# Optimization experiments

Measured on AMD Instinct MI355X. Metric: run time of the kernel, lower is better.

Reference implementation:

```python
import jax, jax.numpy as jnp
import numpy as np

N_USERS = 100_000
N_ITEMS = 50_000
N = N_USERS + N_ITEMS
E = 1_000_000
D = 64          # emb_size
H = 4           # head_num
DH = D // H
L_GT = 2
L_GCN = 2


def setup_inputs() -> dict:
    key = jax.random.key(0)
    ks = jax.random.split(key, 8)
    rows = jax.random.randint(ks[0], (E,), 0, N, dtype=jnp.int32)
    cols = jax.random.randint(ks[1], (E,), 0, N, dtype=jnp.int32)
    vals = jax.random.uniform(ks[2], (E,), dtype=jnp.float32)
    user_emb = jax.random.normal(ks[3], (N_USERS, D), dtype=jnp.float32) * 0.1
    item_emb = jax.random.normal(ks[4], (N_ITEMS, D), dtype=jnp.float32) * 0.1
    scale = 1.0 / np.sqrt(D)  # ~xavier
    Wq = jax.random.normal(ks[5], (L_GT, D, D), dtype=jnp.float32) * scale
    Wk = jax.random.normal(ks[6], (L_GT, D, D), dtype=jnp.float32) * scale
    Wv = jax.random.normal(ks[7], (L_GT, D, D), dtype=jnp.float32) * scale
    return {"rows": rows, "cols": cols, "vals": vals,
            "user_emb": user_emb, "item_emb": item_emb,
            "Wq": Wq, "Wk": Wk, "Wv": Wv}


def _spmm(rows, cols, vals, embeds):
    # torch.spmm(adj, embeds) with adj in COO form -> segment-sum over edges
    return jax.ops.segment_sum(vals[:, None] * embeds[cols], rows, num_segments=N)


def _gt_layer(rows, cols, embeds, wq, wk, wv):
    rowE = embeds[rows]                                   # [E, D] gather
    colE = embeds[cols]                                   # [E, D] gather
    q = (rowE @ wq).reshape(E, H, DH)
    k = (colE @ wk).reshape(E, H, DH)
    v = (colE @ wv).reshape(E, H, DH)
    att = jnp.clip(jnp.einsum('ehd,ehd->eh', q, k), -10.0, 10.0)
    expAtt = jnp.exp(att)                                 # [E, H]
    attNorm = jax.ops.segment_sum(expAtt, rows, num_segments=N)[rows]  # scatter-softmax denom
    att = expAtt / (attNorm + 1e-8)
    res = (att[..., None] * v).reshape(E, D)
    return jax.ops.segment_sum(res, rows, num_segments=N)  # [N, D]


def reference(rows, cols, vals, user_emb, item_emb, Wq, Wk, Wv):
    embeds = jnp.concatenate([user_emb, item_emb], axis=0)  # [N, D]
    embeds_lst = [embeds]
    for l in range(L_GT):
        embeds_lst.append(_gt_layer(rows, cols, embeds_lst[-1], Wq[l], Wk[l], Wv[l]))
    for _ in range(L_GCN):
        embeds_lst.append(_spmm(rows, cols, vals, embeds_lst[-1]))
    out = embeds_lst[0]
    for e in embeds_lst[1:]:
        out = out + e
    return out
```

## Files before the change

kernel.cpp:

```cpp
#include <hip/hip_runtime.h>

#define NUSERS 100000
#define NITEMS 50000
#define NTOT   150000
#define NEDGE  1000000
#define NTILE  9375

typedef unsigned int uint32;
typedef unsigned short ushort16;
typedef __attribute__((ext_vector_type(8))) short short8;
typedef __attribute__((ext_vector_type(4))) float f32x4;

__device__ __forceinline__ unsigned short f2bf(float f) {
  unsigned int u = __float_as_uint(f);
  u += 0x7FFFu + ((u >> 16) & 1u);
  return (unsigned short)(u >> 16);
}
__device__ __forceinline__ uint32 pack2bf(float a, float b) {
  return (uint32)f2bf(a) | ((uint32)f2bf(b) << 16);
}
__device__ __forceinline__ float bf_lo(uint32 u) { return __uint_as_float(u << 16); }
__device__ __forceinline__ float bf_hi(uint32 u) { return __uint_as_float(u & 0xFFFF0000u); }

__global__ void k_init(const float* __restrict__ ue, const float* __restrict__ ie,
                       uint32* __restrict__ embb) {
  int i = blockIdx.x * 256 + threadIdx.x;
  if (i >= NTOT * 16) return;
  float4 v = (i < NUSERS * 16) ? ((const float4*)ue)[i]
                               : ((const float4*)ie)[i - NUSERS * 16];
  uint2 pk;
  pk.x = pack2bf(v.x, v.y);
  pk.y = pack2bf(v.z, v.w);
  ((uint2*)embb)[i] = pk;
}

__global__ void k_wpack(const float* __restrict__ Wq, const float* __restrict__ Wk,
                        const float* __restrict__ Wv, uint32* __restrict__ Wbg) {
  int t = blockIdx.x * 256 + threadIdx.x;
  if (t >= 12288) return;
  int l = t / 6144, rem = t % 6144, mat = rem / 2048, j = rem % 2048;
  int n = j >> 5, k2 = j & 31;
  const float* W = (mat == 0 ? Wq : mat == 1 ? Wk : Wv) + l * 4096;
  Wbg[t] = pack2bf(W[k2 * 128 + n], W[k2 * 128 + 64 + n]);
}

__global__ void k_hist(const int* __restrict__ rows, int* __restrict__ cnt,
                       int* __restrict__ rank) {
  int e = blockIdx.x * 256 + threadIdx.x;
  if (e < NEDGE) rank[e] = atomicAdd(&cnt[rows[e]], 1);
}

__global__ void k_scan1(const int* __restrict__ cnt, int* __restrict__ partial,
                        int* __restrict__ blocksums) {
  __shared__ int s[256];
  int t = threadIdx.x, b = blockIdx.x;
  int base = b * 2048 + t * 8;
  int pre[8]; int sum = 0;
  #pragma unroll
  for (int j = 0; j < 8; ++j) {
    int idx = base + j;
    int x = (idx < NTOT) ? cnt[idx] : 0;
    pre[j] = sum; sum += x;
  }
  s[t] = sum; __syncthreads();
  for (int off = 1; off < 256; off <<= 1) {
    int x = (t >= off) ? s[t - off] : 0;
    __syncthreads(); s[t] += x; __syncthreads();
  }
  int excl = s[t] - sum;
  #pragma unroll
  for (int j = 0; j < 8; ++j) {
    int idx = base + j;
    if (idx < NTOT) partial[idx] = excl + pre[j];
  }
  if (t == 255) blocksums[b] = s[255];
}

__global__ void k_scan2(const int* __restrict__ blocksums, int* __restrict__ blockoffs, int nblk) {
  __shared__ int s[128];
  int t = threadIdx.x;
  int x = (t < nblk) ? blocksums[t] : 0;
  s[t] = x; __syncthreads();
  for (int off = 1; off < 128; off <<= 1) {
    int y = (t >= off) ? s[t - off] : 0;
    __syncthreads(); s[t] += y; __syncthreads();
  }
  if (t < nblk) blockoffs[t] = s[t] - x;
}

__global__ void k_scan3(int* __restrict__ row_ptr, const int* __restrict__ blockoffs) {
  int i = blockIdx.x * 256 + threadIdx.x;
  if (i < NTOT) row_ptr[i] += blockoffs[i >> 11];
  if (i == 0) row_ptr[NTOT] = NEDGE;
}

__global__ void k_fill(const int* __restrict__ rows, const int* __restrict__ cols,
                       const float* __restrict__ vals, const int* __restrict__ rank,
                       const int* __restrict__ row_ptr, uint2* __restrict__ epack) {
  int e = blockIdx.x * 256 + threadIdx.x;
  if (e >= NEDGE) return;
  int r = rows[e];
  int pos = row_ptr[r] + rank[e];
  uint2 pk;
  pk.x = (uint32)cols[e];
  pk.y = __float_as_uint(vals[e]);
  epack[pos] = pk;
}

__global__ void __launch_bounds__(256) k_qkv(const uint32* __restrict__ embb,
    const uint32* __restrict__ Wbg, float* __restrict__ Q, uint32* __restrict__ KVb) {
  __shared__ float scr[4][2][16][68];
  int t = threadIdx.x;
  int wave = t >> 6, lane = t & 63;
  int tile = blockIdx.x * 4 + wave;
  if (tile >= NTILE) return;
  int c = lane & 15, quad = lane >> 4;
  int nodeBase = tile * 16;
  const uint32* arow = embb + (nodeBase + c) * 32 + quad * 4;
  uint4 a0u = *(const uint4*)arow;
  uint4 a1u = *(const uint4*)(arow + 16);
  short8 a0 = *(short8*)&a0u;
  short8 a1 = *(short8*)&a1u;
  float (*SK)[68] = scr[wave][0];
  float (*SV)[68] = scr[wave][1];
  const uint32* wbase = Wbg + c * 32 + quad * 4;
  #pragma unroll
  for (int mat = 0; mat < 3; ++mat) {
    f32x4 acc[4];
    #pragma unroll
    for (int nt = 0; nt < 4; ++nt) acc[nt] = (f32x4){0.f, 0.f, 0.f, 0.f};
    const uint32* wb = wbase + mat * 2048;
    #pragma unroll
    for (int nt = 0; nt < 4; ++nt) {
      uint4 b0u = *(const uint4*)(wb + nt * 512);
      uint4 b1u = *(const uint4*)(wb + nt * 512 + 16);
      short8 b0 = *(short8*)&b0u;
      short8 b1 = *(short8*)&b1u;
      acc[nt] = __builtin_amdgcn_mfma_f32_16x16x32_bf16(a0, b0, acc[nt], 0, 0, 0);
      acc[nt] = __builtin_amdgcn_mfma_f32_16x16x32_bf16(a1, b1, acc[nt], 0, 0, 0);
    }
    float (*S)[68] = (mat == 2) ? SV : SK;
    #pragma unroll
    for (int nt = 0; nt < 4; ++nt)
      #pragma unroll
      for (int r = 0; r < 4; ++r)
        S[quad * 4 + r][nt * 16 + c] = acc[nt][r];
    if (mat == 0) {
      #pragma unroll
      for (int i = 0; i < 4; ++i) {
        int node = i * 4 + quad;
        f32x4 q4 = *(f32x4*)&SK[node][c * 4];
        *(f32x4*)&Q[(nodeBase + node) * 64 + c * 4] = q4;
      }
    } else if (mat == 2) {
      #pragma unroll
      for (int i = 0; i < 4; ++i) {
        int node = i * 4 + quad;
        f32x4 K4 = *(f32x4*)&SK[node][c * 4];
        f32x4 V4 = *(f32x4*)&SV[node][c * 4];
        uint4 o;
        o.x = pack2bf(K4[0], K4[1]);
        o.y = pack2bf(K4[2], K4[3]);
        o.z = pack2bf(V4[0], V4[1]);
        o.w = pack2bf(V4[2], V4[3]);
        *(uint4*)&KVb[(nodeBase + node) * 64 + c * 4] = o;
      }
    }
  }
}

__global__ void __launch_bounds__(256) k_gt(const float* __restrict__ Q,
    const uint32* __restrict__ KVb, const int* __restrict__ row_ptr,
    const uint2* __restrict__ epack, float* __restrict__ emb_out,
    uint32* __restrict__ embb_out) {
  int t = threadIdx.x;
  int n = blockIdx.x * 4 + (t >> 6);
  if (n >= NTOT) return;
  int lane = t & 63;
  int es = lane >> 4;
  int dl = lane & 15;
  float4 q4 = *(const float4*)&Q[n * 64 + dl * 4];
  int s     = __builtin_amdgcn_readfirstlane(row_ptr[n]);
  int e_end = __builtin_amdgcn_readfirstlane(row_ptr[n + 1]);
  int cnt = e_end - s;
  int li = s + lane;
  int cv = (int)epack[li < NEDGE ? li : NEDGE - 1].x;
  float den = 0.f;
  float4 acc = make_float4(0.f, 0.f, 0.f, 0.f);
  #pragma unroll 2
  for (int base = 0; base < cnt; base += 4) {
    int i = base + es;
    int cc;
    if (base < 64) cc = __shfl(cv, i & 63);
    else           cc = (i < cnt) ? (int)epack[s + i].x : 0;
    float ex = 0.f;
    float4 v4 = make_float4(0.f, 0.f, 0.f, 0.f);
    if (i < cnt) {
      uint4 w = *(const uint4*)&KVb[cc * 64 + dl * 4];
      float kx = bf_lo(w.x), ky = bf_hi(w.x);
      float kz = bf_lo(w.y), kw = bf_hi(w.y);
      v4.x = bf_lo(w.z); v4.y = bf_hi(w.z);
      v4.z = bf_lo(w.w); v4.w = bf_hi(w.w);
      float x = q4.x * kx + q4.y * ky + q4.z * kz + q4.w * kw;
      x += __shfl_xor(x, 1);
      x += __shfl_xor(x, 2);
      x = fminf(fmaxf(x, -10.f), 10.f);
      ex = __expf(x);
    }
    den += ex;
    acc.x = fmaf(ex, v4.x, acc.x);
    acc.y = fmaf(ex, v4.y, acc.y);
    acc.z = fmaf(ex, v4.z, acc.z);
    acc.w = fmaf(ex, v4.w, acc.w);
  }
  #pragma unroll
  for (int off = 16; off <= 32; off <<= 1) {
    den  += __shfl_xor(den, off);
    acc.x += __shfl_xor(acc.x, off);
    acc.y += __shfl_xor(acc.y, off);
    acc.z += __shfl_xor(acc.z, off);
    acc.w += __shfl_xor(acc.w, off);
  }
  float inv = 1.f / (den + 1e-8f);
  float4 r = make_float4(acc.x * inv, acc.y * inv, acc.z * inv, acc.w * inv);
  if (es == 0) {
    *(float4*)&emb_out[n * 64 + dl * 4] = r;
  } else if (es == 1) {
    uint2 pk;
    pk.x = pack2bf(r.x, r.y);
    pk.y = pack2bf(r.z, r.w);
    *(uint2*)&embb_out[n * 32 + dl * 2] = pk;
  }
}

template<int FINAL>
__global__ void __launch_bounds__(256) k_gcn(const ushort16* __restrict__ src,
    const int* __restrict__ row_ptr, const uint2* __restrict__ epack,
    float* __restrict__ emb_out, ushort16* __restrict__ embb_out,
    const float* __restrict__ ue, const float* __restrict__ ie,
    const float* __restrict__ add1, const float* __restrict__ add2,
    const float* __restrict__ addG) {
  int t = threadIdx.x;
  int n = blockIdx.x * 4 + (t >> 6);
  if (n >= NTOT) return;
  int lane = t & 63;
  int s     = __builtin_amdgcn_readfirstlane(row_ptr[n]);
  int e_end = __builtin_amdgcn_readfirstlane(row_ptr[n + 1]);
  float a[8];
  #pragma unroll
  for (int j = 0; j < 8; ++j) a[j] = 0.f;
  for (int p = s; p < e_end; p += 8) {
    #pragma unroll
    for (int j = 0; j < 8; ++j) {
      int pj = p + j;
      int pc = (pj < e_end) ? pj : s;
      uint2 ev = epack[pc];
      float w = (pj < e_end) ? __uint_as_float(ev.y) : 0.f;
      int c = (int)ev.x;
      float m = __uint_as_float((uint32)src[c * 64 + lane] << 16);
      a[j] = fmaf(w, m, a[j]);
    }
  }
  float acc = ((a[0] + a[1]) + (a[2] + a[3])) + ((a[4] + a[5]) + (a[6] + a[7]));
  int base = n * 64 + lane;
  if (FINAL) {
    float b = (n < NUSERS) ? ue[base] : ie[base - NUSERS * 64];
    acc += b + add1[base] + add2[base] + addG[base];
    emb_out[base] = acc;
  } else {
    emb_out[base] = acc;
    embb_out[base] = f2bf(acc);
  }
}

extern "C" void kernel_launch(void* const* d_in, const int* in_sizes, int n_in,
                              void* d_out, int out_size, void* d_ws, size_t ws_size,
                              hipStream_t stream) {
  const int*   rows = (const int*)d_in[0];
  const int*   cols = (const int*)d_in[1];
  const float* vals = (const float*)d_in[2];
  const float* ue   = (const float*)d_in[3];
  const float* ie   = (const float*)d_in[4];
  const float* Wq   = (const float*)d_in[5];
  const float* Wk   = (const float*)d_in[6];
  const float* Wv   = (const float*)d_in[7];
  float* out = (float*)d_out;

  char* p = (char*)d_ws;
  auto alloc = [&](size_t b) { char* r = p; p += (b + 255) & ~(size_t)255; return (void*)r; };
  int*   cnt     = (int*)alloc((size_t)NTOT * 4);
  int*   row_ptr = (int*)alloc((size_t)(NTOT + 1) * 4);
  int*   rank    = (int*)alloc((size_t)NEDGE * 4);
  int*   bsums   = (int*)alloc(128 * 4);
  int*   boffs   = (int*)alloc(128 * 4);
  uint2* epack   = (uint2*)alloc((size_t)NEDGE * 8);
  uint32* Wbg  = (uint32*)alloc((size_t)12288 * 4);
  float*  Q    = (float*)alloc((size_t)NTOT * 64 * 4);
  uint32* KVb  = (uint32*)alloc((size_t)NTOT * 64 * 4);
  float*  embA = (float*)alloc((size_t)NTOT * 64 * 4);
  float*  embB = (float*)alloc((size_t)NTOT * 64 * 4);
  uint32* embb0 = (uint32*)alloc((size_t)NTOT * 32 * 4);
  uint32* embb1 = (uint32*)alloc((size_t)NTOT * 32 * 4);

  hipMemsetAsync(cnt, 0, (size_t)NTOT * 4, stream);
  k_hist<<<(NEDGE + 255) / 256, 256, 0, stream>>>(rows, cnt, rank);
  int nblk = (NTOT + 2047) / 2048;
  k_scan1<<<nblk, 256, 0, stream>>>(cnt, row_ptr, bsums);
  k_scan2<<<1, 128, 0, stream>>>(bsums, boffs, nblk);
  k_scan3<<<(NTOT + 255) / 256, 256, 0, stream>>>(row_ptr, boffs);
  k_fill<<<(NEDGE + 255) / 256, 256, 0, stream>>>(rows, cols, vals, rank, row_ptr, epack);
  k_wpack<<<48, 256, 0, stream>>>(Wq, Wk, Wv, Wbg);
  k_init<<<(NTOT * 16 + 255) / 256, 256, 0, stream>>>(ue, ie, embb0);

  k_qkv<<<(NTILE + 3) / 4, 256, 0, stream>>>(embb0, Wbg, Q, KVb);
  k_gt<<<(NTOT + 3) / 4, 256, 0, stream>>>(Q, KVb, row_ptr, epack, embA, embb1);
  k_qkv<<<(NTILE + 3) / 4, 256, 0, stream>>>(embb1, Wbg + 6144, Q, KVb);
  k_gt<<<(NTOT + 3) / 4, 256, 0, stream>>>(Q, KVb, row_ptr, epack, embB, embb0);
  k_gcn<0><<<(NTOT + 3) / 4, 256, 0, stream>>>((const ushort16*)embb0, row_ptr, epack,
                                               Q, (ushort16*)embb1,
                                               nullptr, nullptr, nullptr, nullptr, nullptr);
  k_gcn<1><<<(NTOT + 3) / 4, 256, 0, stream>>>((const ushort16*)embb1, row_ptr, epack,
                                               out, nullptr,
                                               ue, ie, embA, embB, Q);
}
```

Before: 477.5 us.

## Merge setup kernels and keep intermediate embeddings only in bf16

Three setup kernels (bf16 embedding init, weight packing, and the row histogram) are merged into one launch, so two launches go away. The GT and GCN layers no longer write fp32 copies of their outputs. The final GCN kernel reads the layer outputs from bf16 buffers, including the previous GCN output, which is its own input. This cuts global memory writes and reads of fp32 intermediates, but the final sum now uses bf16-rounded layer outputs, which lowers accuracy.

```diff
diff --git a/kernel.cpp b/kernel.cpp
--- a/kernel.cpp
+++ b/kernel.cpp
@@ -7,7 +7,7 @@
 #define NTILE  9375
 
 typedef unsigned int uint32;
-typedef unsigned short ushort16;
+typedef unsigned short bf16u;
 typedef __attribute__((ext_vector_type(8))) short short8;
 typedef __attribute__((ext_vector_type(4))) float f32x4;
 
@@ -21,33 +21,33 @@
 }
 __device__ __forceinline__ float bf_lo(uint32 u) { return __uint_as_float(u << 16); }
 __device__ __forceinline__ float bf_hi(uint32 u) { return __uint_as_float(u & 0xFFFF0000u); }
-
-__global__ void k_init(const float* __restrict__ ue, const float* __restrict__ ie,
-                       uint32* __restrict__ embb) {
-  int i = blockIdx.x * 256 + threadIdx.x;
-  if (i >= NTOT * 16) return;
-  float4 v = (i < NUSERS * 16) ? ((const float4*)ue)[i]
-                               : ((const float4*)ie)[i - NUSERS * 16];
-  uint2 pk;
-  pk.x = pack2bf(v.x, v.y);
-  pk.y = pack2bf(v.z, v.w);
-  ((uint2*)embb)[i] = pk;
-}
-
-__global__ void k_wpack(const float* __restrict__ Wq, const float* __restrict__ Wk,
-                        const float* __restrict__ Wv, uint32* __restrict__ Wbg) {
-  int t = blockIdx.x * 256 + threadIdx.x;
-  if (t >= 12288) return;
-  int l = t / 6144, rem = t % 6144, mat = rem / 2048, j = rem % 2048;
-  int n = j >> 5, k2 = j & 31;
-  const float* W = (mat == 0 ? Wq : mat == 1 ? Wk : Wv) + l * 4096;
-  Wbg[t] = pack2bf(W[k2 * 128 + n], W[k2 * 128 + 64 + n]);
-}
-
-__global__ void k_hist(const int* __restrict__ rows, int* __restrict__ cnt,
-                       int* __restrict__ rank) {
-  int e = blockIdx.x * 256 + threadIdx.x;
-  if (e < NEDGE) rank[e] = atomicAdd(&cnt[rows[e]], 1);
+__device__ __forceinline__ float bf2f(bf16u v) { return __uint_as_float((uint32)v << 16); }
+
+__global__ void k_combo(const float* __restrict__ ue, const float* __restrict__ ie,
+                        uint32* __restrict__ embb,
+                        const float* __restrict__ Wq, const float* __restrict__ Wk,
+                        const float* __restrict__ Wv, uint32* __restrict__ Wbg,
+                        const int* __restrict__ rows, int* __restrict__ cnt,
+                        int* __restrict__ rank) {
+  int b = blockIdx.x, t = threadIdx.x;
+  if (b < 9375) {
+    int i = b * 256 + t;
+    float4 v = (i < NUSERS * 16) ? ((const float4*)ue)[i]
+                                 : ((const float4*)ie)[i - NUSERS * 16];
+    uint2 pk;
+    pk.x = pack2bf(v.x, v.y);
+    pk.y = pack2bf(v.z, v.w);
+    ((uint2*)embb)[i] = pk;
+  } else if (b < 9423) {
+    int i = (b - 9375) * 256 + t;
+    int l = i / 6144, rem = i % 6144, mat = rem / 2048, j = rem % 2048;
+    int n = j >> 5, k2 = j & 31;
+    const float* W = (mat == 0 ? Wq : mat == 1 ? Wk : Wv) + l * 4096;
+    Wbg[i] = pack2bf(W[k2 * 128 + n], W[k2 * 128 + 64 + n]);
+  } else {
+    int e = (b - 9423) * 256 + t;
+    if (e < NEDGE) rank[e] = atomicAdd(&cnt[rows[e]], 1);
+  }
 }
 
 __global__ void k_scan1(const int* __restrict__ cnt, int* __restrict__ partial,
@@ -171,8 +171,7 @@
 
 __global__ void __launch_bounds__(256) k_gt(const float* __restrict__ Q,
     const uint32* __restrict__ KVb, const int* __restrict__ row_ptr,
-    const uint2* __restrict__ epack, float* __restrict__ emb_out,
-    uint32* __restrict__ embb_out) {
+    const uint2* __restrict__ epack, uint32* __restrict__ embb_out) {
   int t = threadIdx.x;
   int n = blockIdx.x * 4 + (t >> 6);
   if (n >= NTOT) return;
@@ -222,30 +221,35 @@
     acc.w += __shfl_xor(acc.w, off);
   }
   float inv = 1.f / (den + 1e-8f);
-  float4 r = make_float4(acc.x * inv, acc.y * inv, acc.z * inv, acc.w * inv);
   if (es == 0) {
-    *(float4*)&emb_out[n * 64 + dl * 4] = r;
-  } else if (es == 1) {
     uint2 pk;
-    pk.x = pack2bf(r.x, r.y);
-    pk.y = pack2bf(r.z, r.w);
+    pk.x = pack2bf(acc.x * inv, acc.y * inv);
+    pk.y = pack2bf(acc.z * inv, acc.w * inv);
     *(uint2*)&embb_out[n * 32 + dl * 2] = pk;
   }
 }
 
 template<int FINAL>
-__global__ void __launch_bounds__(256) k_gcn(const ushort16* __restrict__ src,
+__global__ void __launch_bounds__(256) k_gcn(const bf16u* __restrict__ src,
     const int* __restrict__ row_ptr, const uint2* __restrict__ epack,
-    float* __restrict__ emb_out, ushort16* __restrict__ embb_out,
+    bf16u* __restrict__ embb_out, float* __restrict__ out,
     const float* __restrict__ ue, const float* __restrict__ ie,
-    const float* __restrict__ add1, const float* __restrict__ add2,
-    const float* __restrict__ addG) {
+    const bf16u* __restrict__ add1, const bf16u* __restrict__ add2) {
   int t = threadIdx.x;
   int n = blockIdx.x * 4 + (t >> 6);
   if (n >= NTOT) return;
   int lane = t & 63;
   int s     = __builtin_amdgcn_readfirstlane(row_ptr[n]);
   int e_end = __builtin_amdgcn_readfirstlane(row_ptr[n + 1]);
+  int base = n * 64 + lane;
+  float sum_extra = 0.f;
+  if (FINAL) {
+    float b = (n < NUSERS) ? ue[base] : ie[base - NUSERS * 64];
+    float t1 = bf2f(add1[base]);
+    float t2 = bf2f(add2[base]);
+    float t3 = bf2f(src[base]);
+    sum_extra = (b + t1) + (t2 + t3);
+  }
   float a[8];
   #pragma unroll
   for (int j = 0; j < 8; ++j) a[j] = 0.f;
@@ -257,18 +261,13 @@
       uint2 ev = epack[pc];
       float w = (pj < e_end) ? __uint_as_float(ev.y) : 0.f;
       int c = (int)ev.x;
-      float m = __uint_as_float((uint32)src[c * 64 + lane] << 16);
-      a[j] = fmaf(w, m, a[j]);
+      a[j] = fmaf(w, bf2f(src[c * 64 + lane]), a[j]);
     }
   }
   float acc = ((a[0] + a[1]) + (a[2] + a[3])) + ((a[4] + a[5]) + (a[6] + a[7]));
-  int base = n * 64 + lane;
   if (FINAL) {
-    float b = (n < NUSERS) ? ue[base] : ie[base - NUSERS * 64];
-    acc += b + add1[base] + add2[base] + addG[base];
-    emb_out[base] = acc;
+    out[base] = acc + sum_extra;
   } else {
-    emb_out[base] = acc;
     embb_out[base] = f2bf(acc);
   }
 }
@@ -297,29 +296,27 @@
   uint32* Wbg  = (uint32*)alloc((size_t)12288 * 4);
   float*  Q    = (float*)alloc((size_t)NTOT * 64 * 4);
   uint32* KVb  = (uint32*)alloc((size_t)NTOT * 64 * 4);
-  float*  embA = (float*)alloc((size_t)NTOT * 64 * 4);
-  float*  embB = (float*)alloc((size_t)NTOT * 64 * 4);
-  uint32* embb0 = (uint32*)alloc((size_t)NTOT * 32 * 4);
-  uint32* embb1 = (uint32*)alloc((size_t)NTOT * 32 * 4);
+  uint32* B0   = (uint32*)alloc((size_t)NTOT * 32 * 4);
+  uint32* B1   = (uint32*)alloc((size_t)NTOT * 32 * 4);
+  uint32* B2   = (uint32*)alloc((size_t)NTOT * 32 * 4);
+  uint32* B3   = (uint32*)alloc((size_t)NTOT * 32 * 4);
 
   hipMemsetAsync(cnt, 0, (size_t)NTOT * 4, stream);
-  k_hist<<<(NEDGE + 255) / 256, 256, 0, stream>>>(rows, cnt, rank);
+  k_combo<<<13330, 256, 0, stream>>>(ue, ie, B0, Wq, Wk, Wv, Wbg, rows, cnt, rank);
   int nblk = (NTOT + 2047) / 2048;
   k_scan1<<<nblk, 256, 0, stream>>>(cnt, row_ptr, bsums);
   k_scan2<<<1, 128, 0, stream>>>(bsums, boffs, nblk);
   k_scan3<<<(NTOT + 255) / 256, 256, 0, stream>>>(row_ptr, boffs);
   k_fill<<<(NEDGE + 255) / 256, 256, 0, stream>>>(rows, cols, vals, rank, row_ptr, epack);
-  k_wpack<<<48, 256, 0, stream>>>(Wq, Wk, Wv, Wbg);
-  k_init<<<(NTOT * 16 + 255) / 256, 256, 0, stream>>>(ue, ie, embb0);
-
-  k_qkv<<<(NTILE + 3) / 4, 256, 0, stream>>>(embb0, Wbg, Q, KVb);
-  k_gt<<<(NTOT + 3) / 4, 256, 0, stream>>>(Q, KVb, row_ptr, epack, embA, embb1);
-  k_qkv<<<(NTILE + 3) / 4, 256, 0, stream>>>(embb1, Wbg + 6144, Q, KVb);
-  k_gt<<<(NTOT + 3) / 4, 256, 0, stream>>>(Q, KVb, row_ptr, epack, embB, embb0);
-  k_gcn<0><<<(NTOT + 3) / 4, 256, 0, stream>>>((const ushort16*)embb0, row_ptr, epack,
-                                               Q, (ushort16*)embb1,
-                                               nullptr, nullptr, nullptr, nullptr, nullptr);
-  k_gcn<1><<<(NTOT + 3) / 4, 256, 0, stream>>>((const ushort16*)embb1, row_ptr, epack,
-                                               out, nullptr,
-                                               ue, ie, embA, embB, Q);
-}
+
+  k_qkv<<<(NTILE + 3) / 4, 256, 0, stream>>>(B0, Wbg, Q, KVb);
+  k_gt<<<(NTOT + 3) / 4, 256, 0, stream>>>(Q, KVb, row_ptr, epack, B1);
+  k_qkv<<<(NTILE + 3) / 4, 256, 0, stream>>>(B1, Wbg + 6144, Q, KVb);
+  k_gt<<<(NTOT + 3) / 4, 256, 0, stream>>>(Q, KVb, row_ptr, epack, B2);
+  k_gcn<0><<<(NTOT + 3) / 4, 256, 0, stream>>>((const bf16u*)B2, row_ptr, epack,
+                                               (bf16u*)B3, nullptr,
+                                               nullptr, nullptr, nullptr, nullptr);
+  k_gcn<1><<<(NTOT + 3) / 4, 256, 0, stream>>>((const bf16u*)B3, row_ptr, epack,
+                                               nullptr, out,
+                                               ue, ie, (const bf16u*)B1, (const bf16u*)B2);
+}
```

Measured after the change: 458.1 us. 1.04x faster.
